# Kernel optimization log

Measured on AMD Instinct MI355X. Metric: run time of the kernel, lower is better.

## Reference

```python
import jax, jax.numpy as jnp
import numpy as np

N_NODES = 50000
N_EDGES = 800000
IN_DIM = 128
IN_CH = 64
HIDDEN = 64
OUT_CH = 128
NUM_CLS = 16
NUM_GRAPHS = 512


def setup_inputs() -> dict:
    key = jax.random.key(0)
    ks = jax.random.split(key, 16)
    s = 0.02
    x = jax.random.normal(ks[0], (N_NODES, IN_DIM), jnp.float32)
    edge_index = jax.random.randint(ks[1], (2, N_EDGES), 0, N_NODES, jnp.int64)
    batch = jnp.sort(jax.random.randint(ks[2], (N_NODES,), 0, NUM_GRAPHS, jnp.int64))
    return {
        "x": x,
        "edge_index": edge_index,
        "batch": batch,
        "num_graphs": NUM_GRAPHS,
        "w_stage1": jax.random.normal(ks[3], (IN_DIM, IN_CH), jnp.float32) * s,
        "b_stage1": jnp.zeros((IN_CH,), jnp.float32),
        "rel1_w": jax.random.normal(ks[4], (IN_CH, HIDDEN), jnp.float32) * s,
        "rel1_b": jnp.zeros((HIDDEN,), jnp.float32),
        "root1_w": jax.random.normal(ks[5], (IN_CH, HIDDEN), jnp.float32) * s,
        "rel2_w": jax.random.normal(ks[6], (HIDDEN, 2 * HIDDEN), jnp.float32) * s,
        "rel2_b": jnp.zeros((2 * HIDDEN,), jnp.float32),
        "root2_w": jax.random.normal(ks[7], (HIDDEN, 2 * HIDDEN), jnp.float32) * s,
        "rel3_w": jax.random.normal(ks[8], (2 * HIDDEN, OUT_CH), jnp.float32) * s,
        "rel3_b": jnp.zeros((OUT_CH,), jnp.float32),
        "root3_w": jax.random.normal(ks[9], (2 * HIDDEN, OUT_CH), jnp.float32) * s,
        "lin_w": jax.random.normal(ks[10], (OUT_CH, NUM_CLS), jnp.float32) * s,
        "lin_b": jnp.zeros((NUM_CLS,), jnp.float32),
    }


def graph_conv(x, src, dst, rel_w, rel_b, root_w, n_nodes):
    # PyG GraphConv(aggr='add'): lin_rel(sum_{j in N(i)} x_j) + lin_root(x_i)
    agg = jax.ops.segment_sum(x[src], dst, num_segments=n_nodes)  # [N, in]
    return agg @ rel_w + rel_b + x @ root_w


def reference(x, edge_index, batch, num_graphs,
              w_stage1, b_stage1,
              rel1_w, rel1_b, root1_w,
              rel2_w, rel2_b, root2_w,
              rel3_w, rel3_b, root3_w,
              lin_w, lin_b):
    src, dst = edge_index[0], edge_index[1]
    n = x.shape[0]
    h = x @ w_stage1 + b_stage1                                   # [N, IN_CH]
    h = jax.nn.relu(graph_conv(h, src, dst, rel1_w, rel1_b, root1_w, n))
    h = jax.nn.relu(graph_conv(h, src, dst, rel2_w, rel2_b, root2_w, n))
    h = jax.nn.relu(graph_conv(h, src, dst, rel3_w, rel3_b, root3_w, n))
    # global mean pool over graphs
    sums = jax.ops.segment_sum(h, batch, num_segments=num_graphs)  # [G, OUT_CH]
    cnt = jax.ops.segment_sum(jnp.ones((n,), h.dtype), batch, num_segments=num_graphs)
    pooled = sums / jnp.maximum(cnt, 1.0)[:, None]
    # dropout treated as identity (deterministic eval reference)
    return pooled @ lin_w + lin_b                                  # [G, NUM_CLS]
```

## Files before the change

### kernel.cpp

```cpp
#include <hip/hip_runtime.h>
#include <hip/hip_bf16.h>

#define N_NODES 50000
#define N_EDGES 800000
#define IN_DIM  128
#define IN_CH   64
#define HIDDEN  64
#define OUT_CH  128
#define NUM_CLS 16
#define NUM_G   512
#define NBUK    ((N_NODES + 255) >> 8)
#define BCAP    6144
#define EPB_A   4096

typedef __attribute__((ext_vector_type(8))) short short8;
typedef __attribute__((ext_vector_type(4))) float f32x4;

__device__ inline float bits2f(unsigned short u) {
  unsigned x = (unsigned)u << 16;
  float f;
  __builtin_memcpy(&f, &x, 4);
  return f;
}
__device__ inline unsigned short f2bits(float v) {
  __hip_bfloat16 b = __float2bfloat16(v);
  unsigned short s;
  __builtin_memcpy(&s, &b, 2);
  return s;
}
__device__ inline short8 zero8() {
  short8 z;
#pragma unroll
  for (int i = 0; i < 8; ++i) z[i] = 0;
  return z;
}
__device__ inline void acc2(float& a0, float& a1, unsigned v) {
  a0 += bits2f((unsigned short)v);
  a1 += bits2f((unsigned short)(v >> 16));
}
__device__ inline void accu4(float* a, uint4 v) {
  acc2(a[0], a[1], v.x); acc2(a[2], a[3], v.y);
  acc2(a[4], a[5], v.z); acc2(a[6], a[7], v.w);
}

__global__ __launch_bounds__(256) void k_stage1(
    const float* __restrict__ Ap, const short* __restrict__ Wa,
    const float* __restrict__ bias, unsigned short* __restrict__ outp) {
  constexpr int DIN = 128, DOUT = 64, KT = DIN / 32, CT = DOUT / 16;
  const int wave = threadIdx.x >> 6;
  const int lane = threadIdx.x & 63;
  const int m = lane & 15;
  const int q = lane >> 4;
  const int rbase = blockIdx.x * 128 + wave * 32;

  short8 afr[2][KT];
#pragma unroll
  for (int rt = 0; rt < 2; ++rt) {
    int row = rbase + rt * 16 + m;
    bool ok = row < N_NODES;
#pragma unroll
    for (int kt = 0; kt < KT; ++kt) {
      short8 f = zero8();
      if (ok) {
        const float* ap = Ap + (size_t)row * DIN + kt * 32 + q * 8;
        float4 x0 = *(const float4*)ap;
        float4 x1 = *(const float4*)(ap + 4);
        f[0] = (short)f2bits(x0.x); f[1] = (short)f2bits(x0.y);
        f[2] = (short)f2bits(x0.z); f[3] = (short)f2bits(x0.w);
        f[4] = (short)f2bits(x1.x); f[5] = (short)f2bits(x1.y);
        f[6] = (short)f2bits(x1.z); f[7] = (short)f2bits(x1.w);
      }
      afr[rt][kt] = f;
    }
  }
  for (int ct = 0; ct < CT; ++ct) {
    f32x4 acc0 = {0.f, 0.f, 0.f, 0.f};
    f32x4 acc1 = {0.f, 0.f, 0.f, 0.f};
#pragma unroll
    for (int kt = 0; kt < KT; ++kt) {
      short8 b = *(const short8*)(Wa + ((size_t)(kt * CT + ct) * 64 + lane) * 8);
      acc0 = __builtin_amdgcn_mfma_f32_16x16x32_bf16(afr[0][kt], b, acc0, 0, 0, 0);
      acc1 = __builtin_amdgcn_mfma_f32_16x16x32_bf16(afr[1][kt], b, acc1, 0, 0, 0);
    }
    float bv = bias[ct * 16 + m];
#pragma unroll
    for (int r = 0; r < 4; ++r) {
      int row0 = rbase + q * 4 + r;
      int row1 = row0 + 16;
      if (row0 < N_NODES) outp[(size_t)row0 * DOUT + ct * 16 + m] = f2bits(acc0[r] + bv);
      if (row1 < N_NODES) outp[(size_t)row1 * DOUT + ct * 16 + m] = f2bits(acc1[r] + bv);
    }
  }
}

template <int DIN, int DOUT>
__global__ __launch_bounds__(64) void k_fused(
    const unsigned short* __restrict__ h, const int* __restrict__ esrc,
    const int* __restrict__ off, const short* __restrict__ Wa,
    const short* __restrict__ Wh, const float* __restrict__ bias,
    unsigned short* __restrict__ outp) {
  constexpr int KT = DIN / 32;
  constexpr int CT = DOUT / 16;
  const int lane = threadIdx.x;
  const int m = lane & 15;
  const int q = lane >> 4;
  const int node = blockIdx.x * 16 + m;

  float acc[KT][8];
#pragma unroll
  for (int kt = 0; kt < KT; ++kt)
#pragma unroll
    for (int j = 0; j < 8; ++j) acc[kt][j] = 0.f;
  if (node < N_NODES) {
    int e = off[node], end = off[node + 1];
    const unsigned short* hq = h + q * 8;
    for (; e + 2 <= end; e += 2) {
      int s0 = esrc[e], s1 = esrc[e + 1];
      const unsigned short* r0 = hq + (size_t)s0 * DIN;
      const unsigned short* r1 = hq + (size_t)s1 * DIN;
#pragma unroll
      for (int kt = 0; kt < KT; ++kt) {
        uint4 va = *(const uint4*)(r0 + kt * 32);
        uint4 vb = *(const uint4*)(r1 + kt * 32);
        accu4(acc[kt], va);
        accu4(acc[kt], vb);
      }
    }
    if (e < end) {
      const unsigned short* r0 = hq + (size_t)esrc[e] * DIN;
#pragma unroll
      for (int kt = 0; kt < KT; ++kt)
        accu4(acc[kt], *(const uint4*)(r0 + kt * 32));
    }
  }

  short8 afr[KT], hfr[KT];
#pragma unroll
  for (int kt = 0; kt < KT; ++kt) {
    short8 f;
#pragma unroll
    for (int j = 0; j < 8; ++j) f[j] = (short)f2bits(acc[kt][j]);
    afr[kt] = f;
    hfr[kt] = (node < N_NODES)
                  ? *(const short8*)(h + (size_t)node * DIN + kt * 32 + q * 8)
                  : zero8();
  }

  const int rbase = blockIdx.x * 16;
#pragma unroll
  for (int ct = 0; ct < CT; ++ct) {
    f32x4 c = {0.f, 0.f, 0.f, 0.f};
#pragma unroll
    for (int kt = 0; kt < KT; ++kt) {
      short8 b = *(const short8*)(Wa + ((size_t)(kt * CT + ct) * 64 + lane) * 8);
      c = __builtin_amdgcn_mfma_f32_16x16x32_bf16(afr[kt], b, c, 0, 0, 0);
      short8 bh = *(const short8*)(Wh + ((size_t)(kt * CT + ct) * 64 + lane) * 8);
      c = __builtin_amdgcn_mfma_f32_16x16x32_bf16(hfr[kt], bh, c, 0, 0, 0);
    }
    float bv = bias[ct * 16 + m];
#pragma unroll
    for (int r = 0; r < 4; ++r) {
      int row = rbase + q * 4 + r;
      if (row < N_NODES)
        outp[(size_t)row * DOUT + ct * 16 + m] = f2bits(fmaxf(c[r] + bv, 0.f));
    }
  }
}

template <int DIN, int DOUT>
__device__ inline void pack1(const float* __restrict__ W, short* __restrict__ o,
                             int t) {
  constexpr int CT = DOUT / 16;
  int j = t & 7;
  int lane = (t >> 3) & 63;
  int kc = t >> 9;
  int ct = kc % CT;
  int kt = kc / CT;
  int k = kt * 32 + (lane >> 4) * 8 + j;
  int n = ct * 16 + (lane & 15);
  o[t] = (short)f2bits(W[k * DOUT + n]);
}

__global__ __launch_bounds__(256) void k_packall(
    const float* w1, const float* r1, const float* o1, const float* r2,
    const float* o2, const float* r3, const float* o3,
    short* w1p, short* r1p, short* o1p, short* r2p, short* o2p,
    short* r3p, short* o3p) {
  int b = blockIdx.x, t = threadIdx.x;
  if      (b < 32)  pack1<128, 64>(w1, w1p, (b - 0) * 256 + t);
  else if (b < 48)  pack1<64, 64>(r1, r1p, (b - 32) * 256 + t);
  else if (b < 64)  pack1<64, 64>(o1, o1p, (b - 48) * 256 + t);
  else if (b < 96)  pack1<64, 128>(r2, r2p, (b - 64) * 256 + t);
  else if (b < 128) pack1<64, 128>(o2, o2p, (b - 96) * 256 + t);
  else if (b < 192) pack1<128, 128>(r3, r3p, (b - 128) * 256 + t);
  else              pack1<128, 128>(o3, o3p, (b - 192) * 256 + t);
}

__global__ __launch_bounds__(256) void k_bucketA(const int* __restrict__ src,
    const int* __restrict__ dst, int* __restrict__ bcnt, uint2* __restrict__ bbuf) {
  __shared__ int hist[NBUK], sbase[NBUK], lcur[NBUK];
  const int t = threadIdx.x;
  for (int i = t; i < NBUK; i += 256) { hist[i] = 0; lcur[i] = 0; }
  __syncthreads();
  const int e0 = blockIdx.x * EPB_A;
  int s_[16], d_[16];
  int cnt = 0;
#pragma unroll
  for (int k = 0; k < 16; ++k) {
    int e = e0 + k * 256 + t;
    if (e < N_EDGES) {
      s_[cnt] = src[e]; d_[cnt] = dst[e];
      atomicAdd(&hist[d_[cnt] >> 8], 1);
      cnt++;
    }
  }
  __syncthreads();
  for (int i = t; i < NBUK; i += 256) sbase[i] = atomicAdd(&bcnt[i], hist[i]);
  __syncthreads();
  for (int k = 0; k < cnt; ++k) {
    int b = d_[k] >> 8;
    int pos = sbase[b] + atomicAdd(&lcur[b], 1);
    if (pos < BCAP) bbuf[(size_t)b * BCAP + pos] = make_uint2((unsigned)s_[k], (unsigned)d_[k]);
  }
}

__global__ __launch_bounds__(256) void k_scanb(const int* __restrict__ bcnt,
    int* __restrict__ bbase, int* __restrict__ off) {
  __shared__ int s[256];
  int t = threadIdx.x;
  int v0 = (t < NBUK) ? min(bcnt[t], BCAP) : 0;
  s[t] = v0;
  __syncthreads();
  for (int st = 1; st < 256; st <<= 1) {
    int v = (t >= st) ? s[t - st] : 0;
    __syncthreads();
    s[t] += v;
    __syncthreads();
  }
  if (t < NBUK) bbase[t] = s[t] - v0;
  if (t == NBUK - 1) off[N_NODES] = s[t];
}

__global__ __launch_bounds__(256) void k_bdeg2(const int* __restrict__ bcnt,
    const uint2* __restrict__ bbuf, const int* __restrict__ bbase,
    int* __restrict__ off) {
  __shared__ int cnt[256], s[256];
  const int b = blockIdx.x;
  const int t = threadIdx.x;
  cnt[t] = 0;
  __syncthreads();
  int n = min(bcnt[b], BCAP);
  for (int i = t; i < n; i += 256)
    atomicAdd(&cnt[bbuf[(size_t)b * BCAP + i].y & 255], 1);
  __syncthreads();
  int v0 = cnt[t];
  s[t] = v0;
  __syncthreads();
  for (int st = 1; st < 256; st <<= 1) {
    int v = (t >= st) ? s[t - st] : 0;
    __syncthreads();
    s[t] += v;
    __syncthreads();
  }
  int node = b * 256 + t;
  if (node < N_NODES) off[node] = bbase[b] + s[t] - v0;
}

__global__ __launch_bounds__(256) void k_bscatter(const int* __restrict__ bcnt,
    const uint2* __restrict__ bbuf, const int* __restrict__ off,
    int* __restrict__ esrc) {
  __shared__ int cur[256], soff[256];
  const int b = blockIdx.x;
  cur[threadIdx.x] = 0;
  int node = b * 256 + threadIdx.x;
  soff[threadIdx.x] = (node < N_NODES) ? off[node] : 0;
  __syncthreads();
  int n = min(bcnt[b], BCAP);
  for (int i = threadIdx.x; i < n; i += 256) {
    uint2 p = bbuf[(size_t)b * BCAP + i];
    int l = p.y & 255;
    int r = atomicAdd(&cur[l], 1);
    esrc[soff[l] + r] = (int)p.x;
  }
}

__device__ inline int lbound(const int* __restrict__ a, int n, int v) {
  int lo = 0, hi = n;
  while (lo < hi) {
    int m = (lo + hi) >> 1;
    if (a[m] < v) lo = m + 1; else hi = m;
  }
  return lo;
}

__global__ __launch_bounds__(128) void k_poolhead(const unsigned short* __restrict__ h3,
    const int* __restrict__ batch, const float* __restrict__ lw,
    const float* __restrict__ lb, float* __restrict__ out) {
  __shared__ float sp[128];
  int g = blockIdx.x;
  int t = threadIdx.x;
  int lo = lbound(batch, N_NODES, g);
  int hi = lbound(batch, N_NODES, g + 1);
  float a0 = 0.f, a1 = 0.f, a2 = 0.f, a3 = 0.f;
  int r = lo;
  for (; r + 4 <= hi; r += 4) {
    a0 += bits2f(h3[(size_t)(r + 0) * OUT_CH + t]);
    a1 += bits2f(h3[(size_t)(r + 1) * OUT_CH + t]);
    a2 += bits2f(h3[(size_t)(r + 2) * OUT_CH + t]);
    a3 += bits2f(h3[(size_t)(r + 3) * OUT_CH + t]);
  }
  for (; r < hi; ++r) a0 += bits2f(h3[(size_t)r * OUT_CH + t]);
  float inv = (hi > lo) ? 1.f / (float)(hi - lo) : 0.f;
  sp[t] = ((a0 + a1) + (a2 + a3)) * inv;
  __syncthreads();
  if (t < NUM_CLS) {
    float s = lb[t];
#pragma unroll
    for (int k = 0; k < OUT_CH; ++k) s = fmaf(sp[k], lw[k * NUM_CLS + t], s);
    out[g * NUM_CLS + t] = s;
  }
}

extern "C" void kernel_launch(void* const* d_in, const int* in_sizes, int n_in,
                              void* d_out, int out_size, void* d_ws, size_t ws_size,
                              hipStream_t stream) {
  const float* x      = (const float*)d_in[0];
  const int*   ei     = (const int*)d_in[1];
  const int*   batch  = (const int*)d_in[2];
  const float* w1     = (const float*)d_in[4];
  const float* b1     = (const float*)d_in[5];
  const float* rel1w  = (const float*)d_in[6];
  const float* rel1b  = (const float*)d_in[7];
  const float* root1w = (const float*)d_in[8];
  const float* rel2w  = (const float*)d_in[9];
  const float* rel2b  = (const float*)d_in[10];
  const float* root2w = (const float*)d_in[11];
  const float* rel3w  = (const float*)d_in[12];
  const float* rel3b  = (const float*)d_in[13];
  const float* root3w = (const float*)d_in[14];
  const float* linw   = (const float*)d_in[15];
  const float* linb   = (const float*)d_in[16];
  const int* src = ei;
  const int* dst = ei + N_EDGES;
  float* out = (float*)d_out;

  unsigned short* P = (unsigned short*)d_ws;
  unsigned short* Q = P + (size_t)N_NODES * 128;
  unsigned short* R = Q + (size_t)N_NODES * 128;
  short* WP = (short*)(R + (size_t)N_NODES * 128);
  short* w1p  = WP;
  short* r1p  = w1p + 8192;
  short* o1p  = r1p + 4096;
  short* r2p  = o1p + 4096;
  short* o2p  = r2p + 8192;
  short* r3p  = o2p + 8192;
  short* o3p  = r3p + 16384;
  int* off     = (int*)(o3p + 16384);
  int* bcnt    = off + (N_NODES + 1);
  int* bbase   = bcnt + NBUK;
  int* esrc    = bbase + NBUK + 2;
  uint2* bbuf  = (uint2*)((char*)(esrc + N_EDGES) +
                          ((16 - (((size_t)(esrc + N_EDGES)) & 15)) & 15));

  hipMemsetAsync(bcnt, 0, NBUK * sizeof(int), stream);
  k_bucketA<<<(N_EDGES + EPB_A - 1) / EPB_A, 256, 0, stream>>>(src, dst, bcnt, bbuf);
  k_scanb<<<1, 256, 0, stream>>>(bcnt, bbase, off);
  k_bdeg2<<<NBUK, 256, 0, stream>>>(bcnt, bbuf, bbase, off);
  k_bscatter<<<NBUK, 256, 0, stream>>>(bcnt, bbuf, off, esrc);

  k_packall<<<256, 256, 0, stream>>>(w1, rel1w, root1w, rel2w, root2w, rel3w,
                                     root3w, w1p, r1p, o1p, r2p, o2p, r3p, o3p);

  const int GB = (N_NODES + 127) / 128;
  const int GF = (N_NODES + 15) / 16;

  k_stage1<<<GB, 256, 0, stream>>>(x, w1p, b1, P);
  k_fused<64, 64><<<GF, 64, 0, stream>>>(P, esrc, off, r1p, o1p, rel1b, R);
  k_fused<64, 128><<<GF, 64, 0, stream>>>(R, esrc, off, r2p, o2p, rel2b, Q);
  k_fused<128, 128><<<GF, 64, 0, stream>>>(Q, esrc, off, r3p, o3p, rel3b, P);
  k_poolhead<<<NUM_G, 128, 0, stream>>>(P, batch, linw, linb, out);
}
```

Measured before the change: 254.8 us.

## Split edge aggregation across four waves, merge CSR kernels, shrink stage1 blocks

Each fused GraphConv block now uses four waves that each gather a quarter of every node's neighbour list. The partial sums are reduced through shared memory before wave 0 runs the MFMA epilogue. This is meant to expose more memory-level parallelism in the latency-bound gather, at the cost of LDS traffic, a barrier and three idle waves during the matmul. The degree-count and scatter kernels are merged into one launch, and stage1 now uses one-wave blocks of 16 rows.

```diff
diff --git a/kernel.cpp b/kernel.cpp
--- a/kernel.cpp
+++ b/kernel.cpp
@@ -43,65 +43,63 @@
   acc2(a[4], a[5], v.z); acc2(a[6], a[7], v.w);
 }
 
-__global__ __launch_bounds__(256) void k_stage1(
+__global__ __launch_bounds__(64) void k_stage1(
     const float* __restrict__ Ap, const short* __restrict__ Wa,
     const float* __restrict__ bias, unsigned short* __restrict__ outp) {
   constexpr int DIN = 128, DOUT = 64, KT = DIN / 32, CT = DOUT / 16;
-  const int wave = threadIdx.x >> 6;
-  const int lane = threadIdx.x & 63;
+  const int lane = threadIdx.x;
   const int m = lane & 15;
   const int q = lane >> 4;
-  const int rbase = blockIdx.x * 128 + wave * 32;
-
-  short8 afr[2][KT];
-#pragma unroll
-  for (int rt = 0; rt < 2; ++rt) {
-    int row = rbase + rt * 16 + m;
-    bool ok = row < N_NODES;
-#pragma unroll
-    for (int kt = 0; kt < KT; ++kt) {
-      short8 f = zero8();
-      if (ok) {
-        const float* ap = Ap + (size_t)row * DIN + kt * 32 + q * 8;
-        float4 x0 = *(const float4*)ap;
-        float4 x1 = *(const float4*)(ap + 4);
-        f[0] = (short)f2bits(x0.x); f[1] = (short)f2bits(x0.y);
-        f[2] = (short)f2bits(x0.z); f[3] = (short)f2bits(x0.w);
-        f[4] = (short)f2bits(x1.x); f[5] = (short)f2bits(x1.y);
-        f[6] = (short)f2bits(x1.z); f[7] = (short)f2bits(x1.w);
-      }
-      afr[rt][kt] = f;
-    }
-  }
+  const int row = blockIdx.x * 16 + m;
+  const bool ok = row < N_NODES;
+
+  short8 afr[KT];
+#pragma unroll
+  for (int kt = 0; kt < KT; ++kt) {
+    short8 f = zero8();
+    if (ok) {
+      const float* ap = Ap + (size_t)row * DIN + kt * 32 + q * 8;
+      float4 x0 = *(const float4*)ap;
+      float4 x1 = *(const float4*)(ap + 4);
+      f[0] = (short)f2bits(x0.x); f[1] = (short)f2bits(x0.y);
+      f[2] = (short)f2bits(x0.z); f[3] = (short)f2bits(x0.w);
+      f[4] = (short)f2bits(x1.x); f[5] = (short)f2bits(x1.y);
+      f[6] = (short)f2bits(x1.z); f[7] = (short)f2bits(x1.w);
+    }
+    afr[kt] = f;
+  }
+  const int rbase = blockIdx.x * 16;
+#pragma unroll
   for (int ct = 0; ct < CT; ++ct) {
-    f32x4 acc0 = {0.f, 0.f, 0.f, 0.f};
-    f32x4 acc1 = {0.f, 0.f, 0.f, 0.f};
+    f32x4 c = {0.f, 0.f, 0.f, 0.f};
 #pragma unroll
     for (int kt = 0; kt < KT; ++kt) {
       short8 b = *(const short8*)(Wa + ((size_t)(kt * CT + ct) * 64 + lane) * 8);
-      acc0 = __builtin_amdgcn_mfma_f32_16x16x32_bf16(afr[0][kt], b, acc0, 0, 0, 0);
-      acc1 = __builtin_amdgcn_mfma_f32_16x16x32_bf16(afr[1][kt], b, acc1, 0, 0, 0);
+      c = __builtin_amdgcn_mfma_f32_16x16x32_bf16(afr[kt], b, c, 0, 0, 0);
     }
     float bv = bias[ct * 16 + m];
 #pragma unroll
     for (int r = 0; r < 4; ++r) {
-      int row0 = rbase + q * 4 + r;
-      int row1 = row0 + 16;
-      if (row0 < N_NODES) outp[(size_t)row0 * DOUT + ct * 16 + m] = f2bits(acc0[r] + bv);
-      if (row1 < N_NODES) outp[(size_t)row1 * DOUT + ct * 16 + m] = f2bits(acc1[r] + bv);
+      int ro = rbase + q * 4 + r;
+      if (ro < N_NODES) outp[(size_t)ro * DOUT + ct * 16 + m] = f2bits(c[r] + bv);
     }
   }
 }
 
 template <int DIN, int DOUT>
-__global__ __launch_bounds__(64) void k_fused(
+__global__ __launch_bounds__(256) void k_fused(
     const unsigned short* __restrict__ h, const int* __restrict__ esrc,
     const int* __restrict__ off, const short* __restrict__ Wa,
     const short* __restrict__ Wh, const float* __restrict__ bias,
     unsigned short* __restrict__ outp) {
   constexpr int KT = DIN / 32;
   constexpr int CT = DOUT / 16;
-  const int lane = threadIdx.x;
+  constexpr int NE = KT * 8;
+  __shared__ float lsum[3 * NE * 64];
+
+  const int tid = threadIdx.x;
+  const int wave = tid >> 6;
+  const int lane = tid & 63;
   const int m = lane & 15;
   const int q = lane >> 4;
   const int node = blockIdx.x * 16 + m;
@@ -111,8 +109,11 @@
   for (int kt = 0; kt < KT; ++kt)
 #pragma unroll
     for (int j = 0; j < 8; ++j) acc[kt][j] = 0.f;
+
   if (node < N_NODES) {
-    int e = off[node], end = off[node + 1];
+    int beg = off[node], len = off[node + 1] - beg;
+    int e = beg + (len * wave) / 4;
+    int end = beg + (len * (wave + 1)) / 4;
     const unsigned short* hq = h + q * 8;
     for (; e + 2 <= end; e += 2) {
       int s0 = esrc[e], s1 = esrc[e + 1];
@@ -132,6 +133,25 @@
       for (int kt = 0; kt < KT; ++kt)
         accu4(acc[kt], *(const uint4*)(r0 + kt * 32));
     }
+  }
+
+  if (wave > 0) {
+    float* base = lsum + (size_t)(wave - 1) * NE * 64 + lane;
+#pragma unroll
+    for (int kt = 0; kt < KT; ++kt)
+#pragma unroll
+      for (int j = 0; j < 8; ++j) base[(kt * 8 + j) * 64] = acc[kt][j];
+  }
+  __syncthreads();
+  if (wave != 0) return;
+
+#pragma unroll
+  for (int w = 0; w < 3; ++w) {
+    const float* base = lsum + (size_t)w * NE * 64 + lane;
+#pragma unroll
+    for (int kt = 0; kt < KT; ++kt)
+#pragma unroll
+      for (int j = 0; j < 8; ++j) acc[kt][j] += base[(kt * 8 + j) * 64];
   }
 
   short8 afr[KT], hfr[KT];
@@ -241,10 +261,10 @@
   if (t == NBUK - 1) off[N_NODES] = s[t];
 }
 
-__global__ __launch_bounds__(256) void k_bdeg2(const int* __restrict__ bcnt,
+__global__ __launch_bounds__(256) void k_bfin(const int* __restrict__ bcnt,
     const uint2* __restrict__ bbuf, const int* __restrict__ bbase,
-    int* __restrict__ off) {
-  __shared__ int cnt[256], s[256];
+    int* __restrict__ off, int* __restrict__ esrc) {
+  __shared__ int cnt[256], s[256], soff[256];
   const int b = blockIdx.x;
   const int t = threadIdx.x;
   cnt[t] = 0;
@@ -262,24 +282,16 @@
     s[t] += v;
     __syncthreads();
   }
+  int myoff = bbase[b] + s[t] - v0;
   int node = b * 256 + t;
-  if (node < N_NODES) off[node] = bbase[b] + s[t] - v0;
-}
-
-__global__ __launch_bounds__(256) void k_bscatter(const int* __restrict__ bcnt,
-    const uint2* __restrict__ bbuf, const int* __restrict__ off,
-    int* __restrict__ esrc) {
-  __shared__ int cur[256], soff[256];
-  const int b = blockIdx.x;
-  cur[threadIdx.x] = 0;
-  int node = b * 256 + threadIdx.x;
-  soff[threadIdx.x] = (node < N_NODES) ? off[node] : 0;
-  __syncthreads();
-  int n = min(bcnt[b], BCAP);
-  for (int i = threadIdx.x; i < n; i += 256) {
+  if (node < N_NODES) off[node] = myoff;
+  soff[t] = myoff;
+  cnt[t] = 0;
+  __syncthreads();
+  for (int i = t; i < n; i += 256) {
     uint2 p = bbuf[(size_t)b * BCAP + i];
     int l = p.y & 255;
-    int r = atomicAdd(&cur[l], 1);
+    int r = atomicAdd(&cnt[l], 1);
     esrc[soff[l] + r] = (int)p.x;
   }
 }
@@ -365,18 +377,16 @@
   hipMemsetAsync(bcnt, 0, NBUK * sizeof(int), stream);
   k_bucketA<<<(N_EDGES + EPB_A - 1) / EPB_A, 256, 0, stream>>>(src, dst, bcnt, bbuf);
   k_scanb<<<1, 256, 0, stream>>>(bcnt, bbase, off);
-  k_bdeg2<<<NBUK, 256, 0, stream>>>(bcnt, bbuf, bbase, off);
-  k_bscatter<<<NBUK, 256, 0, stream>>>(bcnt, bbuf, off, esrc);
+  k_bfin<<<NBUK, 256, 0, stream>>>(bcnt, bbuf, bbase, off, esrc);
 
   k_packall<<<256, 256, 0, stream>>>(w1, rel1w, root1w, rel2w, root2w, rel3w,
                                      root3w, w1p, r1p, o1p, r2p, o2p, r3p, o3p);
 
-  const int GB = (N_NODES + 127) / 128;
   const int GF = (N_NODES + 15) / 16;
 
-  k_stage1<<<GB, 256, 0, stream>>>(x, w1p, b1, P);
-  k_fused<64, 64><<<GF, 64, 0, stream>>>(P, esrc, off, r1p, o1p, rel1b, R);
-  k_fused<64, 128><<<GF, 64, 0, stream>>>(R, esrc, off, r2p, o2p, rel2b, Q);
-  k_fused<128, 128><<<GF, 64, 0, stream>>>(Q, esrc, off, r3p, o3p, rel3b, P);
+  k_stage1<<<GF, 64, 0, stream>>>(x, w1p, b1, P);
+  k_fused<64, 64><<<GF, 256, 0, stream>>>(P, esrc, off, r1p, o1p, rel1b, R);
+  k_fused<64, 128><<<GF, 256, 0, stream>>>(R, esrc, off, r2p, o2p, rel2b, Q);
+  k_fused<128, 128><<<GF, 256, 0, stream>>>(Q, esrc, off, r3p, o3p, rel3b, P);
   k_poolhead<<<NUM_G, 128, 0, stream>>>(P, batch, linw, linb, out);
 }
```

After: 283.1 us. +11.1%, slower.
